# Kernel optimization log

Hardware: AMD Instinct MI355X
Metric: run time of the kernel (lower is better)

The kernel has to match this reference:

```python
import jax
import jax.numpy as jnp
import numpy as np
from jax import lax

B, L, A, C = 32, 128, 64, 128  # batch, length, n_agents, channels (in == out)
KT = 3                          # temporal kernel size, padding (KT-1)//2 keeps length


def setup_inputs() -> dict:
    key = jax.random.key(0)
    k1, k2, k3 = jax.random.split(key, 3)
    x = jax.random.normal(k1, (B, L, A, C), dtype=jnp.float32)
    # Conv2d weight [out_ch, in_ch, kt, 1] and bias, kaiming-ish scale
    W = jax.random.normal(k2, (C, C, KT, 1), dtype=jnp.float32) * (1.0 / np.sqrt(C * KT))
    b = jax.random.normal(k3, (C,), dtype=jnp.float32) * 0.01
    return {"x": x, "W": W, "b": b}


def reference(x, W, b):
    # x: [B, L, A, C] -> [B, C, L, A] (torch NCHW layout with H=time, W=agents)
    length, n_agents = x.shape[1], x.shape[2]
    xc = jnp.transpose(x, (0, 3, 1, 2))
    res = xc  # residual is identity (input_dim == output_dim, t_stride == 1)
    pad_t = (KT - 1) // 2
    y = lax.conv_general_dilated(
        xc, W,
        window_strides=(1, 1),
        padding=[(pad_t, pad_t), (0, 0)],
        dimension_numbers=("NCHW", "OIHW", "NCHW"),
    ) + b[None, :, None, None]  # [B, C, L, A]
    # Dense graph g[t,a,t',a'] = 1 iff t==t' or a==a'.  einsum('ncv,vw->ncw', x, g)
    # is exactly: sum over same time (all agents) + sum over same agent (all times) - self.
    agent_sum = jnp.sum(y, axis=3, keepdims=True)  # [B, C, L, 1]
    time_sum = jnp.sum(y, axis=2, keepdims=True)   # [B, C, 1, A]
    scale = (length + n_agents - 2) ** 0.5
    g = (agent_sum + time_sum - y) / scale
    out = jax.nn.relu(g + res)
    return jnp.transpose(out, (0, 2, 3, 1))  # [B, L, A, C]
```

## Files before the change

### kernel.cpp

```cpp
#include <hip/hip_runtime.h>
#include <stdint.h>


typedef __attribute__((ext_vector_type(8))) short bf16x8;
typedef __attribute__((ext_vector_type(4))) float f32x4;

__device__ __forceinline__ uint32_t f2bf(float f) {
    union { float f; uint32_t u; } v; v.f = f;
    return (v.u + 0x7FFFu + ((v.u >> 16) & 1u)) >> 16;
}
__device__ __forceinline__ float bf2f(uint32_t h) {
    union { uint32_t u; float f; } v; v.u = h << 16; return v.f;
}
__device__ __forceinline__ uint32_t pk2(float lo, float hi) {
    return f2bf(lo) | (f2bf(hi) << 16);
}
__device__ __forceinline__ void gll16(const void* g, void* l) {
    __builtin_amdgcn_global_load_lds((const __attribute__((address_space(1))) void*)g,
                                     (__attribute__((address_space(3))) void*)l, 16, 0, 0);
}

__global__ __launch_bounds__(256) void prep_kernel(
    const float* __restrict__ x, uint16_t* __restrict__ x16, uint16_t* __restrict__ xa16,
    const float* __restrict__ W, uint16_t* __restrict__ wp)
{
    const int tid = threadIdx.x;
    const int bid = blockIdx.x;
    if (bid >= 4160) {
        int o = (bid - 4160) * 256 + tid;
        int i = o & 7, lane = (o >> 3) & 63, nt = (o >> 9) & 7, ks = (o >> 12) & 3, d = o >> 14;
        int ci = ks * 32 + (lane >> 4) * 8 + i;
        int co = nt * 16 + (lane & 15);
        wp[o] = (uint16_t)f2bf(W[(co * 128 + ci) * 3 + d]);
        return;
    }
    const int b = bid / 130, tp = bid - b * 130;
    uint16_t* xo = x16 + (size_t)bid * 8192;
    if (tp == 0 || tp == 129) {
        const uint4 z = make_uint4(0, 0, 0, 0);
        #pragma unroll
        for (int k = 0; k < 4; ++k) *(uint4*)(xo + tid * 32 + k * 8) = z;
        if (tid < 16) *(uint4*)(xa16 + (size_t)bid * 128 + tid * 8) = z;
        return;
    }
    const int t = tp - 1;
    const int ci4 = (tid & 31) * 4, ag = tid >> 5;
    const float* xr = x + (size_t)(b * 128 + t) * 8192;
    float4 part = make_float4(0.f, 0.f, 0.f, 0.f);
    #pragma unroll
    for (int r = 0; r < 8; ++r) {
        const int a = ag * 8 + r;
        const float4 v = *(const float4*)(xr + a * 128 + ci4);
        part.x += v.x; part.y += v.y; part.z += v.z; part.w += v.w;
        uint2 p; p.x = pk2(v.x, v.y); p.y = pk2(v.z, v.w);
        *(uint2*)(xo + a * 128 + ci4) = p;
    }
    __shared__ float red[8][128];
    *(float4*)&red[ag][ci4] = part;
    __syncthreads();
    if (tid < 128) {
        float s = 0.f;
        #pragma unroll
        for (int i = 0; i < 8; ++i) s += red[i][tid];
        xa16[(size_t)bid * 128 + tid] = (uint16_t)f2bf(s);
    }
}

__global__ __launch_bounds__(256) void xt_kernel(
    const uint16_t* __restrict__ x16, float* __restrict__ xt)
{
    const int tid = threadIdx.x, bid = blockIdx.x;
    const int a = bid & 63, b = bid >> 6;
    const int ci8 = (tid & 15) * 8, tg = tid >> 4;
    const uint16_t* base = x16 + ((size_t)(b * 130 + 1 + tg) * 64 + a) * 128 + ci8;
    float s[8];
    #pragma unroll
    for (int j = 0; j < 8; ++j) s[j] = 0.f;
    #pragma unroll
    for (int r = 0; r < 8; ++r) {
        const uint4 v = *(const uint4*)(base + (size_t)r * 16 * 8192);
        s[0] += bf2f(v.x & 0xFFFFu); s[1] += bf2f(v.x >> 16);
        s[2] += bf2f(v.y & 0xFFFFu); s[3] += bf2f(v.y >> 16);
        s[4] += bf2f(v.z & 0xFFFFu); s[5] += bf2f(v.z >> 16);
        s[6] += bf2f(v.w & 0xFFFFu); s[7] += bf2f(v.w >> 16);
    }
    __shared__ float red[16][128];
    *(float4*)&red[tg][ci8]     = make_float4(s[0], s[1], s[2], s[3]);
    *(float4*)&red[tg][ci8 + 4] = make_float4(s[4], s[5], s[6], s[7]);
    __syncthreads();
    if (tid < 128) {
        float v = 0.f;
        #pragma unroll
        for (int i = 0; i < 16; ++i) v += red[i][tid];
        xt[(size_t)bid * 128 + tid] = v;
    }
}

__global__ __launch_bounds__(256, 2) void sums_kernel(
    const uint16_t* __restrict__ xa16, const float* __restrict__ xt,
    const uint16_t* __restrict__ x16, const uint16_t* __restrict__ wp,
    const float* __restrict__ bias, float* __restrict__ asum, float* __restrict__ tsum)
{
    __shared__ __align__(16) uint16_t slab[130 * 128];
    const int tid = threadIdx.x;
    const int lane = tid & 63, wid = tid >> 6;
    const int wm = wid >> 1, wn = wid & 1;
    const int lr = lane & 15, lg = lane >> 4;
    f32x4 acc[4][4];
    #pragma unroll
    for (int mi = 0; mi < 4; ++mi)
        #pragma unroll
        for (int ni = 0; ni < 4; ++ni) acc[mi][ni] = (f32x4)0.f;

    if (blockIdx.x < 32) {
        const int b = blockIdx.x;
        #pragma unroll
        for (int it = 0; it < 9; ++it) {
            const int gg = it * 256 + tid;
            if (gg < 2080) {
                const int row = gg >> 4, sp = gg & 15;
                const int sl = sp ^ (row & 7);
                *(uint4*)(slab + gg * 8) =
                    *(const uint4*)(xa16 + (size_t)(b * 130 + row) * 128 + sl * 8);
            }
        }
        __syncthreads();
        #pragma unroll
        for (int g = 0; g < 4; ++g)
            #pragma unroll
            for (int d = 0; d < 3; ++d) {
                bf16x8 bq[4], af[4];
                #pragma unroll
                for (int ni = 0; ni < 4; ++ni)
                    bq[ni] = *(const bf16x8*)(wp + (size_t)((((d * 4 + g) * 8) + wn * 4 + ni) * 64 + lane) * 8);
                #pragma unroll
                for (int mi = 0; mi < 4; ++mi) {
                    const int row = wm * 64 + mi * 16 + lr + d;
                    af[mi] = *(const bf16x8*)(slab + row * 128 + ((g * 4 + lg) ^ (row & 7)) * 8);
                }
                #pragma unroll
                for (int mi = 0; mi < 4; ++mi)
                    #pragma unroll
                    for (int ni = 0; ni < 4; ++ni)
                        acc[mi][ni] = __builtin_amdgcn_mfma_f32_16x16x32_bf16(af[mi], bq[ni], acc[mi][ni], 0, 0, 0);
            }
        #pragma unroll
        for (int ni = 0; ni < 4; ++ni) {
            const int col = wn * 64 + ni * 16 + lr;
            const float bv = 64.f * bias[col];
            #pragma unroll
            for (int mi = 0; mi < 4; ++mi)
                #pragma unroll
                for (int j = 0; j < 4; ++j) {
                    const int t = wm * 64 + mi * 16 + lg * 4 + j;
                    asum[((size_t)b * 128 + t) * 128 + col] = acc[mi][ni][j] + bv;
                }
        }
        return;
    }

    const int bid = blockIdx.x - 32;
    const int r = tid >> 1, h = tid & 1;
    const int grow = bid * 128 + r, sb = grow >> 6, sa = grow & 63;
    #pragma unroll
    for (int d = 0; d < 3; ++d) {
        {
            const float* Sp = xt + (size_t)grow * 128 + h * 64;
            const uint16_t* Ep = x16 + ((size_t)(sb * 130 + (d == 0 ? 128 : 1)) * 64 + sa) * 128 + h * 64;
            #pragma unroll
            for (int k = 0; k < 8; ++k) {
                float4 f0 = *(const float4*)(Sp + k * 8);
                float4 f1 = *(const float4*)(Sp + k * 8 + 4);
                if (d != 1) {
                    const uint4 e = *(const uint4*)(Ep + k * 8);
                    f0.x -= bf2f(e.x & 0xFFFFu); f0.y -= bf2f(e.x >> 16);
                    f0.z -= bf2f(e.y & 0xFFFFu); f0.w -= bf2f(e.y >> 16);
                    f1.x -= bf2f(e.z & 0xFFFFu); f1.y -= bf2f(e.z >> 16);
                    f1.z -= bf2f(e.w & 0xFFFFu); f1.w -= bf2f(e.w >> 16);
                }
                uint4 o;
                o.x = pk2(f0.x, f0.y); o.y = pk2(f0.z, f0.w);
                o.z = pk2(f1.x, f1.y); o.w = pk2(f1.z, f1.w);
                const int sl = h * 8 + k;
                *(uint4*)(slab + r * 128 + (sl ^ (r & 7)) * 8) = o;
            }
        }
        __syncthreads();
        #pragma unroll
        for (int g = 0; g < 4; ++g) {
            bf16x8 bq[4], af[4];
            #pragma unroll
            for (int ni = 0; ni < 4; ++ni)
                bq[ni] = *(const bf16x8*)(wp + (size_t)((((d * 4 + g) * 8) + wn * 4 + ni) * 64 + lane) * 8);
            #pragma unroll
            for (int mi = 0; mi < 4; ++mi) {
                const int row = wm * 64 + mi * 16 + lr;
                af[mi] = *(const bf16x8*)(slab + row * 128 + ((g * 4 + lg) ^ (row & 7)) * 8);
            }
            #pragma unroll
            for (int mi = 0; mi < 4; ++mi)
                #pragma unroll
                for (int ni = 0; ni < 4; ++ni)
                    acc[mi][ni] = __builtin_amdgcn_mfma_f32_16x16x32_bf16(af[mi], bq[ni], acc[mi][ni], 0, 0, 0);
        }
        __syncthreads();
    }
    #pragma unroll
    for (int ni = 0; ni < 4; ++ni) {
        const int col = wn * 64 + ni * 16 + lr;
        const float bv = 128.f * bias[col];
        #pragma unroll
        for (int mi = 0; mi < 4; ++mi)
            #pragma unroll
            for (int j = 0; j < 4; ++j) {
                const int rg = bid * 128 + wm * 64 + mi * 16 + lg * 4 + j;
                tsum[(size_t)rg * 128 + col] = acc[mi][ni][j] + bv;
            }
    }
}

__global__ __launch_bounds__(512, 4) void conv_kernel(
    const uint16_t* __restrict__ x16, const uint16_t* __restrict__ wp,
    const float* __restrict__ bias, const float* __restrict__ asum,
    const float* __restrict__ tsum, float* __restrict__ out)
{
    __shared__ __align__(16) uint16_t slab[256 * 128];
    const int tid = threadIdx.x, bid = blockIdx.x;
    const int b = bid >> 6, t0 = (bid & 63) * 2;
    const int lane = tid & 63, wid = tid >> 6;
    const int lr = lane & 15, lg = lane >> 4;

    #pragma unroll
    for (int k = 0; k < 8; ++k) {
        const int row = wid * 32 + k * 4 + lg;
        const int sl = lr ^ (row & 7);
        const uint16_t* src = x16 +
            ((size_t)((b * 130 + t0 + (row >> 6)) * 64 + (row & 63))) * 128 + sl * 8;
        gll16(src, slab + wid * 4096 + k * 512);
    }
    __syncthreads();

    const int wm = wid >> 2, wn = wid & 3;
    f32x4 acc[4][2];
    #pragma unroll
    for (int mi = 0; mi < 4; ++mi)
        #pragma unroll
        for (int ni = 0; ni < 2; ++ni) acc[mi][ni] = (f32x4)0.f;

    const int sx = lr & 7;
    #pragma unroll
    for (int g = 0; g < 4; ++g)
        #pragma unroll
        for (int d = 0; d < 3; ++d) {
            bf16x8 bq[2], af[4];
            #pragma unroll
            for (int ni = 0; ni < 2; ++ni)
                bq[ni] = *(const bf16x8*)(wp + (size_t)((((d * 4 + g) * 8) + wn * 2 + ni) * 64 + lane) * 8);
            #pragma unroll
            for (int mi = 0; mi < 4; ++mi) {
                const int row = (wm + d) * 64 + mi * 16 + lr;
                af[mi] = *(const bf16x8*)(slab + row * 128 + ((g * 4 + lg) ^ sx) * 8);
            }
            #pragma unroll
            for (int mi = 0; mi < 4; ++mi)
                #pragma unroll
                for (int ni = 0; ni < 2; ++ni)
                    acc[mi][ni] = __builtin_amdgcn_mfma_f32_16x16x32_bf16(af[mi], bq[ni], acc[mi][ni], 0, 0, 0);
        }
    __syncthreads();

    #pragma unroll
    for (int ni = 0; ni < 2; ++ni) {
        const int col = wn * 32 + ni * 16 + lr;
        const float bv = bias[col];
        #pragma unroll
        for (int mi = 0; mi < 4; ++mi)
            #pragma unroll
            for (int j = 0; j < 4; ++j) {
                const int ro = wm * 64 + mi * 16 + lg * 4 + j;
                const int rmap = ro + ((ro & 64) << 1);
                slab[rmap * 128 + (col ^ ((ro & 7) << 3))] = (uint16_t)f2bf(acc[mi][ni][j] + bv);
            }
    }
    __syncthreads();

    {
        const float inv = 0.07254762501100116f;
        const int cg = tid & 15, rb = tid >> 4;
        #pragma unroll
        for (int j = 0; j < 4; ++j) {
            const int ro = j * 32 + rb;
            const int t = t0 + (ro >> 6), a = ro & 63;
            const int rmap = ro + ((ro & 64) << 1);
            const uint4 yv = *(const uint4*)(slab + rmap * 128 + ((cg * 8) ^ ((ro & 7) << 3)));
            const uint4 xv = *(const uint4*)(slab + (ro + 64) * 128 + (cg ^ (ro & 7)) * 8);
            const float* ap = asum + ((size_t)(b * 128 + t)) * 128 + cg * 8;
            const float* tp = tsum + ((size_t)(b * 64 + a)) * 128 + cg * 8;
            const float4 as0 = *(const float4*)ap, as1 = *(const float4*)(ap + 4);
            const float4 ts0 = *(const float4*)tp, ts1 = *(const float4*)(tp + 4);
            float yy[8], xx[8];
            yy[0] = bf2f(yv.x & 0xFFFFu); yy[1] = bf2f(yv.x >> 16);
            yy[2] = bf2f(yv.y & 0xFFFFu); yy[3] = bf2f(yv.y >> 16);
            yy[4] = bf2f(yv.z & 0xFFFFu); yy[5] = bf2f(yv.z >> 16);
            yy[6] = bf2f(yv.w & 0xFFFFu); yy[7] = bf2f(yv.w >> 16);
            xx[0] = bf2f(xv.x & 0xFFFFu); xx[1] = bf2f(xv.x >> 16);
            xx[2] = bf2f(xv.y & 0xFFFFu); xx[3] = bf2f(xv.y >> 16);
            xx[4] = bf2f(xv.z & 0xFFFFu); xx[5] = bf2f(xv.z >> 16);
            xx[6] = bf2f(xv.w & 0xFFFFu); xx[7] = bf2f(xv.w >> 16);
            const float av[8] = {as0.x, as0.y, as0.z, as0.w, as1.x, as1.y, as1.z, as1.w};
            const float tv[8] = {ts0.x, ts0.y, ts0.z, ts0.w, ts1.x, ts1.y, ts1.z, ts1.w};
            float o[8];
            #pragma unroll
            for (int i = 0; i < 8; ++i) {
                const float gg = (av[i] + tv[i] - yy[i]) * inv + xx[i];
                o[i] = gg > 0.f ? gg : 0.f;
            }
            float* op = out + ((size_t)((b * 128 + t) * 64 + a)) * 128 + cg * 8;
            *(float4*)op       = make_float4(o[0], o[1], o[2], o[3]);
            *(float4*)(op + 4) = make_float4(o[4], o[5], o[6], o[7]);
        }
    }
}

extern "C" void kernel_launch(void* const* d_in, const int* in_sizes, int n_in,
                              void* d_out, int out_size, void* d_ws, size_t ws_size,
                              hipStream_t stream) {
    const float* x    = (const float*)d_in[0];
    const float* W    = (const float*)d_in[1];
    const float* bias = (const float*)d_in[2];
    float* out = (float*)d_out;

    char* ws = (char*)d_ws;
    uint16_t* x16  = (uint16_t*)(ws);
    uint16_t* wp   = (uint16_t*)(ws + 68157440);
    uint16_t* xa16 = (uint16_t*)(ws + 68157440 + 98304);
    float* xt      = (float*)(ws + 68157440 + 98304 + 1064960);
    float* asum    = (float*)(ws + 68157440 + 98304 + 1064960 + 1048576);
    float* tsum    = (float*)(ws + 68157440 + 98304 + 1064960 + 1048576 + 2097152);

    prep_kernel <<<4352, 256, 0, stream>>>(x, x16, xa16, W, wp);
    xt_kernel   <<<2048, 256, 0, stream>>>(x16, xt);
    sums_kernel <<<48,   256, 0, stream>>>(xa16, xt, x16, wp, bias, asum, tsum);
    conv_kernel <<<2048, 512, 0, stream>>>(x16, wp, bias, asum, tsum, out);
}
```

Before: 131.1 us.

## Shrink conv tile to one time step for higher occupancy and XCD swizzle

Each conv block now processes a single time step with all 8 waves splitting output channels, using a 192-row LDS slab instead of 256. This lowers LDS per block so launch bounds can allow 6 blocks per CU, and block IDs are remapped across XCDs for better L2 locality. In exchange, the temporal halo is reloaded more often (3 input rows per output row instead of 2 per 1), increasing global read traffic.

```diff
diff --git a/kernel.cpp b/kernel.cpp
--- a/kernel.cpp
+++ b/kernel.cpp
@@ -219,67 +219,59 @@
     }
 }
 
-__global__ __launch_bounds__(512, 4) void conv_kernel(
+__global__ __launch_bounds__(512, 6) void conv_kernel(
     const uint16_t* __restrict__ x16, const uint16_t* __restrict__ wp,
     const float* __restrict__ bias, const float* __restrict__ asum,
     const float* __restrict__ tsum, float* __restrict__ out)
 {
-    __shared__ __align__(16) uint16_t slab[256 * 128];
-    const int tid = threadIdx.x, bid = blockIdx.x;
-    const int b = bid >> 6, t0 = (bid & 63) * 2;
+    __shared__ __align__(16) uint16_t slab[192 * 128];
+    const int tid = threadIdx.x;
+    const int raw = blockIdx.x;
+    const int bid = (raw & 7) * 512 + (raw >> 3);
+    const int b = bid >> 7, t = bid & 127;
     const int lane = tid & 63, wid = tid >> 6;
     const int lr = lane & 15, lg = lane >> 4;
 
     #pragma unroll
-    for (int k = 0; k < 8; ++k) {
-        const int row = wid * 32 + k * 4 + lg;
+    for (int k = 0; k < 6; ++k) {
+        const int row = wid * 24 + k * 4 + lg;
         const int sl = lr ^ (row & 7);
         const uint16_t* src = x16 +
-            ((size_t)((b * 130 + t0 + (row >> 6)) * 64 + (row & 63))) * 128 + sl * 8;
-        gll16(src, slab + wid * 4096 + k * 512);
-    }
-    __syncthreads();
-
-    const int wm = wid >> 2, wn = wid & 3;
-    f32x4 acc[4][2];
-    #pragma unroll
-    for (int mi = 0; mi < 4; ++mi)
-        #pragma unroll
-        for (int ni = 0; ni < 2; ++ni) acc[mi][ni] = (f32x4)0.f;
-
-    const int sx = lr & 7;
+            ((size_t)((b * 130 + t + (row >> 6)) * 64 + (row & 63))) * 128 + sl * 8;
+        gll16(src, slab + wid * 3072 + k * 512);
+    }
+    __syncthreads();
+
+    f32x4 acc[4];
+    #pragma unroll
+    for (int mi = 0; mi < 4; ++mi) acc[mi] = (f32x4)0.f;
+
     #pragma unroll
     for (int g = 0; g < 4; ++g)
         #pragma unroll
         for (int d = 0; d < 3; ++d) {
-            bf16x8 bq[2], af[4];
-            #pragma unroll
-            for (int ni = 0; ni < 2; ++ni)
-                bq[ni] = *(const bf16x8*)(wp + (size_t)((((d * 4 + g) * 8) + wn * 2 + ni) * 64 + lane) * 8);
+            bf16x8 bq, af[4];
+            bq = *(const bf16x8*)(wp + (size_t)((((d * 4 + g) * 8) + wid) * 64 + lane) * 8);
             #pragma unroll
             for (int mi = 0; mi < 4; ++mi) {
-                const int row = (wm + d) * 64 + mi * 16 + lr;
-                af[mi] = *(const bf16x8*)(slab + row * 128 + ((g * 4 + lg) ^ sx) * 8);
+                const int row = d * 64 + mi * 16 + lr;
+                af[mi] = *(const bf16x8*)(slab + row * 128 + ((g * 4 + lg) ^ (row & 7)) * 8);
             }
             #pragma unroll
             for (int mi = 0; mi < 4; ++mi)
-                #pragma unroll
-                for (int ni = 0; ni < 2; ++ni)
-                    acc[mi][ni] = __builtin_amdgcn_mfma_f32_16x16x32_bf16(af[mi], bq[ni], acc[mi][ni], 0, 0, 0);
-        }
-    __syncthreads();
-
-    #pragma unroll
-    for (int ni = 0; ni < 2; ++ni) {
-        const int col = wn * 32 + ni * 16 + lr;
+                acc[mi] = __builtin_amdgcn_mfma_f32_16x16x32_bf16(af[mi], bq, acc[mi], 0, 0, 0);
+        }
+    __syncthreads();
+
+    {
+        const int col = wid * 16 + lr;
         const float bv = bias[col];
         #pragma unroll
         for (int mi = 0; mi < 4; ++mi)
             #pragma unroll
             for (int j = 0; j < 4; ++j) {
-                const int ro = wm * 64 + mi * 16 + lg * 4 + j;
-                const int rmap = ro + ((ro & 64) << 1);
-                slab[rmap * 128 + (col ^ ((ro & 7) << 3))] = (uint16_t)f2bf(acc[mi][ni][j] + bv);
+                const int a = mi * 16 + lg * 4 + j;
+                slab[a * 128 + (col ^ ((a & 7) << 3))] = (uint16_t)f2bf(acc[mi][j] + bv);
             }
     }
     __syncthreads();
@@ -287,16 +279,15 @@
     {
         const float inv = 0.07254762501100116f;
         const int cg = tid & 15, rb = tid >> 4;
-        #pragma unroll
-        for (int j = 0; j < 4; ++j) {
-            const int ro = j * 32 + rb;
-            const int t = t0 + (ro >> 6), a = ro & 63;
-            const int rmap = ro + ((ro & 64) << 1);
-            const uint4 yv = *(const uint4*)(slab + rmap * 128 + ((cg * 8) ^ ((ro & 7) << 3)));
-            const uint4 xv = *(const uint4*)(slab + (ro + 64) * 128 + (cg ^ (ro & 7)) * 8);
-            const float* ap = asum + ((size_t)(b * 128 + t)) * 128 + cg * 8;
+        const float* ap = asum + ((size_t)(b * 128 + t)) * 128 + cg * 8;
+        const float4 as0 = *(const float4*)ap, as1 = *(const float4*)(ap + 4);
+        const float av[8] = {as0.x, as0.y, as0.z, as0.w, as1.x, as1.y, as1.z, as1.w};
+        #pragma unroll
+        for (int j = 0; j < 2; ++j) {
+            const int a = j * 32 + rb;
+            const uint4 yv = *(const uint4*)(slab + a * 128 + ((cg * 8) ^ ((a & 7) << 3)));
+            const uint4 xv = *(const uint4*)(slab + (a + 64) * 128 + ((cg * 8) ^ ((a & 7) << 3)));
             const float* tp = tsum + ((size_t)(b * 64 + a)) * 128 + cg * 8;
-            const float4 as0 = *(const float4*)ap, as1 = *(const float4*)(ap + 4);
             const float4 ts0 = *(const float4*)tp, ts1 = *(const float4*)(tp + 4);
             float yy[8], xx[8];
             yy[0] = bf2f(yv.x & 0xFFFFu); yy[1] = bf2f(yv.x >> 16);
@@ -307,7 +298,6 @@
             xx[2] = bf2f(xv.y & 0xFFFFu); xx[3] = bf2f(xv.y >> 16);
             xx[4] = bf2f(xv.z & 0xFFFFu); xx[5] = bf2f(xv.z >> 16);
             xx[6] = bf2f(xv.w & 0xFFFFu); xx[7] = bf2f(xv.w >> 16);
-            const float av[8] = {as0.x, as0.y, as0.z, as0.w, as1.x, as1.y, as1.z, as1.w};
             const float tv[8] = {ts0.x, ts0.y, ts0.z, ts0.w, ts1.x, ts1.y, ts1.z, ts1.w};
             float o[8];
             #pragma unroll
@@ -341,5 +331,5 @@
     prep_kernel <<<4352, 256, 0, stream>>>(x, x16, xa16, W, wp);
     xt_kernel   <<<2048, 256, 0, stream>>>(x16, xt);
     sums_kernel <<<48,   256, 0, stream>>>(xa16, xt, x16, wp, bias, asum, tsum);
-    conv_kernel <<<2048, 512, 0, stream>>>(x16, wp, bias, asum, tsum, out);
-}
+    conv_kernel <<<4096, 512, 0, stream>>>(x16, wp, bias, asum, tsum, out);
+}
```

After: 117.7 us. -10.2%, faster.
